# Kernel optimization log

Measured on AMD Instinct MI355X. Metric: run time of the kernel, lower is better.

## Reference

```python
import jax, jax.numpy as jnp
import numpy as np

N_NODES = 500_000
N_FEAT = 125          # embedding dim; cat with pos(3) -> 128
HIDDEN = 128
OUT_DIM = 64
N_TYPES = 100
N_GRAPHS = 4096


def setup_inputs() -> dict:
    key = jax.random.key(0)
    ks = jax.random.split(key, 10)
    pos = jax.random.normal(ks[0], (N_NODES, 3), dtype=jnp.float32)
    z = jax.random.randint(ks[1], (N_NODES,), 0, N_TYPES)
    batch = jnp.sort(jax.random.randint(ks[2], (N_NODES,), 0, N_GRAPHS))
    emb = jax.random.normal(ks[3], (N_TYPES, N_FEAT), dtype=jnp.float32)
    s1 = 1.0 / np.sqrt(N_FEAT + 3)
    s2 = 1.0 / np.sqrt(HIDDEN)
    W1 = jax.random.normal(ks[4], (N_FEAT + 3, HIDDEN), dtype=jnp.float32) * s1
    b1 = jnp.zeros((HIDDEN,), dtype=jnp.float32)
    W2 = jax.random.normal(ks[5], (HIDDEN, HIDDEN), dtype=jnp.float32) * s2
    b2 = jnp.zeros((HIDDEN,), dtype=jnp.float32)
    W3 = jax.random.normal(ks[6], (HIDDEN, OUT_DIM), dtype=jnp.float32) * s2
    b3 = jnp.zeros((OUT_DIM,), dtype=jnp.float32)
    return {"pos": pos, "z": z, "batch": batch, "emb": emb,
            "W1": W1, "b1": b1, "W2": W2, "b2": b2, "W3": W3, "b3": b3}


def reference(pos, z, batch, emb, W1, b1, W2, b2, W3, b3):
    # embed node types and concat with 3D positions  -> [N, 128]
    x = jnp.concatenate([pos, emb[z]], axis=-1)
    # two equivariant-transformer layers (per-node transform) + relu
    x = jax.nn.relu(x @ W1 + b1)   # [N, H]
    x = jax.nn.relu(x @ W2 + b2)   # [N, H]
    # output head
    x = x @ W3 + b3                # [N, O]
    # global mean pool per graph
    s = jax.ops.segment_sum(x, batch, num_segments=N_GRAPHS)                    # [G, O]
    cnt = jax.ops.segment_sum(jnp.ones((x.shape[0], 1), x.dtype), batch,
                              num_segments=N_GRAPHS)                            # [G, 1]
    return s / jnp.maximum(cnt, 1.0)
```

## Files before the change

kernel.cpp:

```cpp
#include <hip/hip_runtime.h>
#include <hip/hip_bf16.h>

#define N_NODES 500000
#define N_FEAT 125
#define HID 128
#define OUTD 64
#define N_GRAPHS 4096
#define N_TYPES 100
#define WTILE 32
#define NTILES32 (N_NODES / WTILE)
#define NBLOCKS 512
#define NWAVES 8
#define WPAD 136

typedef float f32x4 __attribute__((ext_vector_type(4)));
typedef short s16x8 __attribute__((ext_vector_type(8)));
typedef short s16x4 __attribute__((ext_vector_type(4)));

#define OFF_T 0
#define SZ_T (N_TYPES * WPAD * 2)
#define OFF_W2 (OFF_T + SZ_T)
#define OFF_W3K (OFF_W2 + HID * WPAD * 2)
#define OFF_B2 (OFF_W3K + 4 * 8 * 64 * 8)
#define OFF_W1 (OFF_B2 + HID * 4)
#define LDS_BYTES (OFF_W1 + 3 * HID * 4)

#define WS_GSUM 0
#define WS_GCNT ((size_t)N_GRAPHS * OUTD * 4)
#define WS_T    (WS_GCNT + (size_t)N_GRAPHS * 4)
#define WS_ZERO WS_T
#define WS_ZERO_V4 (WS_ZERO / 16)

__device__ __forceinline__ unsigned short f2bf(float f) {
  union { float f; unsigned u; } v; v.f = f;
  unsigned r = v.u + 0x7FFFu + ((v.u >> 16) & 1u);
  return (unsigned short)(r >> 16);
}
__device__ __forceinline__ float bf2f(unsigned short u) {
  union { unsigned u; float f; } v; v.u = ((unsigned)u) << 16;
  return v.f;
}
__device__ __forceinline__ unsigned pk2bf(float a, float b) {
  __hip_bfloat162 h = __float22bfloat162_rn(float2{a, b});
  union { __hip_bfloat162 h; unsigned u; } v; v.h = h;
  return v.u;
}
__device__ __forceinline__ s16x4 u2frag(uint2 v) {
  union { uint2 u; s16x4 s; } c; c.u = v; return c.s;
}

extern "C" __global__ void gnn_prep(const float* __restrict__ emb,
                                    const float* __restrict__ W1,
                                    const float* __restrict__ b1,
                                    unsigned short* __restrict__ Tg,
                                    f32x4* __restrict__ wsz)
{
  const int j = threadIdx.x;
  const int tid = blockIdx.x * 128 + j;
  for (int i = tid; i < WS_ZERO_V4; i += 256 * 128)
    wsz[i] = (f32x4){0.f, 0.f, 0.f, 0.f};
  const int g = blockIdx.x;
  if (g < N_TYPES) {
    float acc = b1[j];
    const float* er = emb + g * N_FEAT;
    for (int k = 0; k < N_FEAT; ++k)
      acc = fmaf(er[k], W1[(3 + k) * HID + j], acc);
    Tg[g * HID + j] = f2bf(acc);
  }
}

extern "C" __global__ void __launch_bounds__(512, 4)
gnn_main(const float* __restrict__ pos, const int* __restrict__ z,
         const int* __restrict__ batch, const unsigned short* __restrict__ Tg,
         const float* __restrict__ W1, const float* __restrict__ W2,
         const float* __restrict__ b2, const float* __restrict__ W3,
         float* __restrict__ gsum, int* __restrict__ gcnt)
{
  extern __shared__ char lds[];
  unsigned short* Tl  = (unsigned short*)(lds + OFF_T);
  unsigned short* w2t = (unsigned short*)(lds + OFF_W2);
  uint2* w3k = (uint2*)(lds + OFF_W3K);
  float* bias2 = (float*)(lds + OFF_B2);
  float* w1l   = (float*)(lds + OFF_W1);

  const int t = threadIdx.x;

  for (int i = t; i < N_TYPES * HID; i += 512) {
    int g = i >> 7, f = i & 127;
    Tl[g * WPAD + f] = Tg[i];
  }
  for (int i = t; i < HID * HID; i += 512) {
    int k = i >> 7, n = i & 127;
    w2t[n * WPAD + k] = f2bf(W2[i]);
  }
  for (int i = t; i < 4 * 8 * 64; i += 512) {
    int ob = i >> 9, rest = i & 511;
    int oi = rest >> 6, ln = rest & 63;
    int q = ln >> 4, l = ln & 15;
    int f0 = oi * 16 + q * 4, o = ob * 16 + l;
    uint2 v;
    v.x = pk2bf(W3[(f0 + 0) * OUTD + o], W3[(f0 + 1) * OUTD + o]);
    v.y = pk2bf(W3[(f0 + 2) * OUTD + o], W3[(f0 + 3) * OUTD + o]);
    w3k[i] = v;
  }
  if (t < HID) bias2[t] = b2[t];
  if (t < 3 * HID) w1l[t] = W1[t];

  const int wave = t >> 6, lane = t & 63, quad = lane >> 4, l15 = lane & 15;

  __syncthreads();

  const int gwave = blockIdx.x * NWAVES + wave;

  for (int tile = gwave; tile < NTILES32; tile += NBLOCKS * NWAVES) {
    const int base = tile * WTILE;

    const int id0 = batch[base + l15];
    const int id1 = batch[base + 16 + l15];

    s16x8 a[2][4];
    {
      float px[2], py[2], pz[2];
      const unsigned short* Tr[2];
      #pragma unroll
      for (int m = 0; m < 2; ++m) {
        const int node = base + m * 16 + l15;
        const int zi = z[node];
        px[m] = pos[node * 3]; py[m] = pos[node * 3 + 1]; pz[m] = pos[node * 3 + 2];
        Tr[m] = Tl + zi * WPAD;
      }
      #pragma unroll
      for (int k = 0; k < 4; ++k) {
        float w1s[3][8];
        #pragma unroll
        for (int c = 0; c < 3; ++c) {
          *(f32x4*)&w1s[c][0] = *(const f32x4*)(w1l + c * HID + k * 32 + quad * 8);
          *(f32x4*)&w1s[c][4] = *(const f32x4*)(w1l + c * HID + k * 32 + quad * 8 + 4);
        }
        #pragma unroll
        for (int m = 0; m < 2; ++m) {
          s16x8 tf = *(const s16x8*)(Tr[m] + k * 32 + quad * 8);
          s16x8 fr;
          #pragma unroll
          for (int j = 0; j < 8; j += 2) {
            float v0 = bf2f((unsigned short)tf[j])
                     + px[m] * w1s[0][j] + py[m] * w1s[1][j] + pz[m] * w1s[2][j];
            float v1 = bf2f((unsigned short)tf[j + 1])
                     + px[m] * w1s[0][j + 1] + py[m] * w1s[1][j + 1] + pz[m] * w1s[2][j + 1];
            ((unsigned*)&fr)[j >> 1] = pk2bf(fmaxf(v0, 0.f), fmaxf(v1, 0.f));
          }
          a[m][k] = fr;
        }
      }
    }

    uint2 pb[8][2];
    __builtin_amdgcn_s_setprio(1);
    #pragma unroll
    for (int oi = 0; oi < 8; ++oi) {
      f32x4 c0 = {}, c1 = {};
      #pragma unroll
      for (int k = 0; k < 4; ++k) {
        s16x8 w = *(const s16x8*)(w2t + (oi * 16 + l15) * WPAD + k * 32 + quad * 8);
        c0 = __builtin_amdgcn_mfma_f32_16x16x32_bf16(w, a[0][k], c0, 0, 0, 0);
        c1 = __builtin_amdgcn_mfma_f32_16x16x32_bf16(w, a[1][k], c1, 0, 0, 0);
      }
      const int f0 = oi * 16 + quad * 4;
      f32x4 bv = *(const f32x4*)(bias2 + f0);
      pb[oi][0].x = pk2bf(fmaxf(c0[0] + bv[0], 0.f), fmaxf(c0[1] + bv[1], 0.f));
      pb[oi][0].y = pk2bf(fmaxf(c0[2] + bv[2], 0.f), fmaxf(c0[3] + bv[3], 0.f));
      pb[oi][1].x = pk2bf(fmaxf(c1[0] + bv[0], 0.f), fmaxf(c1[1] + bv[1], 0.f));
      pb[oi][1].y = pk2bf(fmaxf(c1[2] + bv[2], 0.f), fmaxf(c1[3] + bv[3], 0.f));
    }
    __builtin_amdgcn_s_setprio(0);

    f32x4 acc3[4][2] = {};
    __builtin_amdgcn_s_setprio(1);
    #pragma unroll
    for (int ob = 0; ob < 4; ++ob)
      #pragma unroll
      for (int oi = 0; oi < 8; ++oi) {
        s16x4 wa = u2frag(w3k[(ob * 8 + oi) * 64 + lane]);
        acc3[ob][0] = __builtin_amdgcn_mfma_f32_16x16x16bf16_1k(
            wa, u2frag(pb[oi][0]), acc3[ob][0], 0, 0, 0);
        acc3[ob][1] = __builtin_amdgcn_mfma_f32_16x16x16bf16_1k(
            wa, u2frag(pb[oi][1]), acc3[ob][1], 0, 0, 0);
      }
    __builtin_amdgcn_s_setprio(0);

    {
      int done = 0;
      while (done < WTILE) {
        const int srcv = (done < 16) ? id0 : id1;
        const int g = __builtin_amdgcn_readlane(srcv, done & 15);
        const bool m0 = (id0 == g), m1 = (id1 == g);
        float red[4][4];
        #pragma unroll
        for (int ob = 0; ob < 4; ++ob)
          #pragma unroll
          for (int r = 0; r < 4; ++r)
            red[ob][r] = (m0 ? acc3[ob][0][r] : 0.f) + (m1 ? acc3[ob][1][r] : 0.f);
        #pragma unroll
        for (int s = 1; s <= 8; s <<= 1)
          #pragma unroll
          for (int ob = 0; ob < 4; ++ob)
            #pragma unroll
            for (int r = 0; r < 4; ++r)
              red[ob][r] += __shfl_xor(red[ob][r], s, 64);
        const int cnt = (int)((__popcll(__ballot(m0)) + __popcll(__ballot(m1))) >> 2);
        if (l15 == 0) {
          #pragma unroll
          for (int ob = 0; ob < 4; ++ob)
            #pragma unroll
            for (int r = 0; r < 4; ++r)
              atomicAdd(&gsum[g * OUTD + ob * 16 + quad * 4 + r], red[ob][r]);
        }
        if (lane == 0) atomicAdd(&gcnt[g], cnt);
        done += cnt;
      }
    }
  }
}

extern "C" __global__ void gnn_finalize(const float* __restrict__ gsum,
                                        const int* __restrict__ gcnt,
                                        const float* __restrict__ b3,
                                        float* __restrict__ out)
{
  int i = blockIdx.x * 256 + threadIdx.x;
  if (i < N_GRAPHS * OUTD) {
    int g = i >> 6, o = i & 63;
    int c = gcnt[g];
    out[i] = (c > 0) ? (gsum[i] / (float)c + b3[o]) : 0.f;
  }
}

extern "C" void kernel_launch(void* const* d_in, const int* in_sizes, int n_in,
                              void* d_out, int out_size, void* d_ws, size_t ws_size,
                              hipStream_t stream) {
  const float* pos  = (const float*)d_in[0];
  const int*   z    = (const int*)d_in[1];
  const int*   batch= (const int*)d_in[2];
  const float* emb  = (const float*)d_in[3];
  const float* W1   = (const float*)d_in[4];
  const float* b1   = (const float*)d_in[5];
  const float* W2   = (const float*)d_in[6];
  const float* b2   = (const float*)d_in[7];
  const float* W3   = (const float*)d_in[8];
  const float* b3   = (const float*)d_in[9];

  float* gsum = (float*)d_ws;
  int*   gcnt = (int*)((char*)d_ws + WS_GCNT);
  unsigned short* Tg = (unsigned short*)((char*)d_ws + WS_T);

  hipLaunchKernelGGL(gnn_prep, dim3(256), dim3(HID), 0, stream,
                     emb, W1, b1, Tg, (f32x4*)d_ws);

  hipFuncSetAttribute((const void*)gnn_main,
                      hipFuncAttributeMaxDynamicSharedMemorySize, LDS_BYTES);
  hipLaunchKernelGGL(gnn_main, dim3(NBLOCKS), dim3(512), LDS_BYTES, stream,
                     pos, z, batch, Tg, W1, W2, b2, W3, gsum, gcnt);
  hipLaunchKernelGGL(gnn_finalize, dim3((N_GRAPHS * OUTD + 255) / 256), dim3(256), 0, stream,
                     gsum, gcnt, b3, (float*)d_out);
}
```

Measured before the change: 158.5 us.

## Process 64-node tiles per wave to amortize weight loads and atomics

Each wave now handles 64 nodes (four 16-row fragments) instead of 32, so every W2/W3 fragment read from LDS feeds four MFMAs rather than two. Each graph segment run also spans more nodes, so fewer reduction passes and global atomics are issued per node. The final 32-node remainder is handled with a flag and a clamped node index. In exchange, accumulator and fragment register use roughly doubles, and launch bounds and block count are halved to 2 blocks per CU, which lowers occupancy and latency hiding.

Measured after the change: 132.9 us (median of 2 runs). -16.1%, faster.

```diff
diff --git a/kernel.cpp b/kernel.cpp
--- a/kernel.cpp
+++ b/kernel.cpp
@@ -7,9 +7,8 @@
 #define OUTD 64
 #define N_GRAPHS 4096
 #define N_TYPES 100
-#define WTILE 32
-#define NTILES32 (N_NODES / WTILE)
-#define NBLOCKS 512
+#define NPAIRS 7813
+#define NBLOCKS 256
 #define NWAVES 8
 #define WPAD 136
 
@@ -69,7 +68,7 @@
   }
 }
 
-extern "C" __global__ void __launch_bounds__(512, 4)
+extern "C" __global__ void __launch_bounds__(512, 2)
 gnn_main(const float* __restrict__ pos, const int* __restrict__ z,
          const int* __restrict__ batch, const unsigned short* __restrict__ Tg,
          const float* __restrict__ W1, const float* __restrict__ W2,
@@ -112,19 +111,26 @@
 
   const int gwave = blockIdx.x * NWAVES + wave;
 
-  for (int tile = gwave; tile < NTILES32; tile += NBLOCKS * NWAVES) {
-    const int base = tile * WTILE;
-
-    const int id0 = batch[base + l15];
-    const int id1 = batch[base + 16 + l15];
-
-    s16x8 a[2][4];
+  for (int pair = gwave; pair < NPAIRS; pair += NBLOCKS * NWAVES) {
+    const int base = pair * 64;
+    const bool has2 = (pair != NPAIRS - 1);
+
+    int id0 = batch[base + l15];
+    int id1 = batch[base + 16 + l15];
+    int id2 = -1, id3 = -1;
+    if (has2) {
+      id2 = batch[base + 32 + l15];
+      id3 = batch[base + 48 + l15];
+    }
+
+    s16x8 a[4][4];
     {
-      float px[2], py[2], pz[2];
-      const unsigned short* Tr[2];
-      #pragma unroll
-      for (int m = 0; m < 2; ++m) {
-        const int node = base + m * 16 + l15;
+      float px[4], py[4], pz[4];
+      const unsigned short* Tr[4];
+      #pragma unroll
+      for (int m = 0; m < 4; ++m) {
+        int node = base + m * 16 + l15;
+        node = node < N_NODES ? node : N_NODES - 1;
         const int zi = z[node];
         px[m] = pos[node * 3]; py[m] = pos[node * 3 + 1]; pz[m] = pos[node * 3 + 2];
         Tr[m] = Tl + zi * WPAD;
@@ -138,7 +144,7 @@
           *(f32x4*)&w1s[c][4] = *(const f32x4*)(w1l + c * HID + k * 32 + quad * 8 + 4);
         }
         #pragma unroll
-        for (int m = 0; m < 2; ++m) {
+        for (int m = 0; m < 4; ++m) {
           s16x8 tf = *(const s16x8*)(Tr[m] + k * 32 + quad * 8);
           s16x8 fr;
           #pragma unroll
@@ -154,52 +160,58 @@
       }
     }
 
-    uint2 pb[8][2];
+    uint2 pb[8][4];
     __builtin_amdgcn_s_setprio(1);
     #pragma unroll
     for (int oi = 0; oi < 8; ++oi) {
-      f32x4 c0 = {}, c1 = {};
+      f32x4 c[4] = {};
       #pragma unroll
       for (int k = 0; k < 4; ++k) {
         s16x8 w = *(const s16x8*)(w2t + (oi * 16 + l15) * WPAD + k * 32 + quad * 8);
-        c0 = __builtin_amdgcn_mfma_f32_16x16x32_bf16(w, a[0][k], c0, 0, 0, 0);
-        c1 = __builtin_amdgcn_mfma_f32_16x16x32_bf16(w, a[1][k], c1, 0, 0, 0);
+        #pragma unroll
+        for (int m = 0; m < 4; ++m)
+          c[m] = __builtin_amdgcn_mfma_f32_16x16x32_bf16(w, a[m][k], c[m], 0, 0, 0);
       }
       const int f0 = oi * 16 + quad * 4;
       f32x4 bv = *(const f32x4*)(bias2 + f0);
-      pb[oi][0].x = pk2bf(fmaxf(c0[0] + bv[0], 0.f), fmaxf(c0[1] + bv[1], 0.f));
-      pb[oi][0].y = pk2bf(fmaxf(c0[2] + bv[2], 0.f), fmaxf(c0[3] + bv[3], 0.f));
-      pb[oi][1].x = pk2bf(fmaxf(c1[0] + bv[0], 0.f), fmaxf(c1[1] + bv[1], 0.f));
-      pb[oi][1].y = pk2bf(fmaxf(c1[2] + bv[2], 0.f), fmaxf(c1[3] + bv[3], 0.f));
+      #pragma unroll
+      for (int m = 0; m < 4; ++m) {
+        pb[oi][m].x = pk2bf(fmaxf(c[m][0] + bv[0], 0.f), fmaxf(c[m][1] + bv[1], 0.f));
+        pb[oi][m].y = pk2bf(fmaxf(c[m][2] + bv[2], 0.f), fmaxf(c[m][3] + bv[3], 0.f));
+      }
     }
     __builtin_amdgcn_s_setprio(0);
 
-    f32x4 acc3[4][2] = {};
+    f32x4 acc3[4][4] = {};
     __builtin_amdgcn_s_setprio(1);
     #pragma unroll
     for (int ob = 0; ob < 4; ++ob)
       #pragma unroll
       for (int oi = 0; oi < 8; ++oi) {
         s16x4 wa = u2frag(w3k[(ob * 8 + oi) * 64 + lane]);
-        acc3[ob][0] = __builtin_amdgcn_mfma_f32_16x16x16bf16_1k(
-            wa, u2frag(pb[oi][0]), acc3[ob][0], 0, 0, 0);
-        acc3[ob][1] = __builtin_amdgcn_mfma_f32_16x16x16bf16_1k(
-            wa, u2frag(pb[oi][1]), acc3[ob][1], 0, 0, 0);
+        #pragma unroll
+        for (int m = 0; m < 4; ++m)
+          acc3[ob][m] = __builtin_amdgcn_mfma_f32_16x16x16bf16_1k(
+              wa, u2frag(pb[oi][m]), acc3[ob][m], 0, 0, 0);
       }
     __builtin_amdgcn_s_setprio(0);
 
     {
+      const int NT = has2 ? 64 : 32;
       int done = 0;
-      while (done < WTILE) {
-        const int srcv = (done < 16) ? id0 : id1;
+      while (done < NT) {
+        const int sel = done >> 4;
+        int srcv = (sel & 2) ? ((sel & 1) ? id3 : id2)
+                             : ((sel & 1) ? id1 : id0);
         const int g = __builtin_amdgcn_readlane(srcv, done & 15);
-        const bool m0 = (id0 == g), m1 = (id1 == g);
+        const bool m0 = (id0 == g), m1 = (id1 == g), m2 = (id2 == g), m3 = (id3 == g);
         float red[4][4];
         #pragma unroll
         for (int ob = 0; ob < 4; ++ob)
           #pragma unroll
           for (int r = 0; r < 4; ++r)
-            red[ob][r] = (m0 ? acc3[ob][0][r] : 0.f) + (m1 ? acc3[ob][1][r] : 0.f);
+            red[ob][r] = (m0 ? acc3[ob][0][r] : 0.f) + (m1 ? acc3[ob][1][r] : 0.f)
+                       + (m2 ? acc3[ob][2][r] : 0.f) + (m3 ? acc3[ob][3][r] : 0.f);
         #pragma unroll
         for (int s = 1; s <= 8; s <<= 1)
           #pragma unroll
@@ -207,7 +219,8 @@
             #pragma unroll
             for (int r = 0; r < 4; ++r)
               red[ob][r] += __shfl_xor(red[ob][r], s, 64);
-        const int cnt = (int)((__popcll(__ballot(m0)) + __popcll(__ballot(m1))) >> 2);
+        const int cnt = (int)((__popcll(__ballot(m0)) + __popcll(__ballot(m1)) +
+                               __popcll(__ballot(m2)) + __popcll(__ballot(m3))) >> 2);
         if (l15 == 0) {
           #pragma unroll
           for (int ob = 0; ob < 4; ++ob)
```
